# Kernel tuning notes

Hardware: AMD Instinct MI355X
Metric: run time of the kernel (lower is better)

Reference implementation:

```python
import jax, jax.numpy as jnp
import numpy as np

B, S, D_IN, D_H = 16, 4096, 512, 512

def setup_inputs() -> dict:
    key = jax.random.key(0)
    ks = jax.random.split(key, 8)
    inp = {
        "input": jax.random.normal(ks[0], (B, D_IN), dtype=jnp.float32),
        "context": jax.random.normal(ks[1], (B, S, D_IN), dtype=jnp.float32),
        "mask": jax.random.bernoulli(ks[2], 0.2, (B, S)),
        # parameters (torch nn.Linear layout: W [out,in], b [out])
        "W_in": jax.random.normal(ks[3], (D_H, D_IN), dtype=jnp.float32) / np.sqrt(D_IN),
        "b_in": jax.random.normal(ks[4], (D_H,), dtype=jnp.float32) * 0.01,
        "W_ctx": jax.random.normal(ks[5], (D_H, D_IN), dtype=jnp.float32) / np.sqrt(D_IN),
        "b_ctx": jax.random.normal(ks[6], (D_H,), dtype=jnp.float32) * 0.01,
        "v": jax.random.normal(ks[7], (D_H,), dtype=jnp.float32),
    }
    return inp


def reference(input, context, mask, W_in, b_in, W_ctx, b_ctx, v):
    # inp: [B, H] projected decoder state
    inp = input @ W_in.T + b_in
    # ctx: [B, S, H] projected context (this is what the torch code matmuls
    # with the softmax weights, i.e. hidden lives in hidden_dim space)
    ctx = context @ W_ctx.T + b_ctx
    # additive (Bahdanau) scores: v . tanh(inp + ctx) -> [B, S]
    scores = jnp.einsum("h,bsh->bs", v, jnp.tanh(inp[:, None, :] + ctx))
    # masked positions get -inf so they receive zero softmax weight
    scores = jnp.where(mask, -jnp.inf, scores)
    attn = jax.nn.softmax(scores, axis=-1)  # [B, S]
    # weighted sum of projected context: [B, H]
    hidden = jnp.einsum("bsh,bs->bh", ctx, attn)
    return hidden, attn
```

## Files before the change

### kernel.cpp

```cpp
#include <hip/hip_runtime.h>
#include <hip/hip_bf16.h>

#define B_  16
#define S_  4096
#define DIN 512
#define DH  512

typedef _Float16 f16x8 __attribute__((ext_vector_type(8)));
typedef float    f32x4 __attribute__((ext_vector_type(4)));


__device__ __forceinline__ float fast_tanh(float x) {
    float e = __expf(2.f * x);
    return 1.f - 2.f * __builtin_amdgcn_rcpf(e + 1.f);
}

__device__ __forceinline__ void gload_lds16(const void* g, void* l) {
    __builtin_amdgcn_global_load_lds(
        (const __attribute__((address_space(1))) void*)g,
        (__attribute__((address_space(3))) void*)l, 16, 0, 0);
}

__device__ __forceinline__ int mask_at(const void* mask, int isByte, int idx) {
    return isByte ? (int)((const unsigned char*)mask)[idx]
                  : ((const int*)mask)[idx];
}

__global__ void prep_kernel(const float* __restrict__ input,
                            const float* __restrict__ W_in,
                            const float* __restrict__ b_in,
                            const float* __restrict__ W_ctx,
                            const float* __restrict__ b_ctx,
                            const void*  __restrict__ mask,
                            _Float16* __restrict__ W16,
                            float* __restrict__ addv,
                            float* __restrict__ zeroRegion,
                            int* __restrict__ maskflag) {
    int blk = blockIdx.x;
    int tid = threadIdx.x;
    if (blk < 256) {
        int base = blk * 1024 + tid * 4;
        float4 wv = *(const float4*)(W_ctx + base);
        union { _Float16 f[4]; ushort4 u; } cv;
        cv.f[0] = (_Float16)wv.x; cv.f[1] = (_Float16)wv.y;
        cv.f[2] = (_Float16)wv.z; cv.f[3] = (_Float16)wv.w;
        *(ushort4*)(W16 + base) = cv.u;
    } else if (blk < 288) {
        int t = blk - 256;
        int b = t >> 1;
        int h = ((t & 1) << 8) + tid;
        __shared__ float inrow[DIN];
        inrow[tid]       = input[b * DIN + tid];
        inrow[tid + 256] = input[b * DIN + tid + 256];
        __syncthreads();
        const float* wr = W_in + (size_t)h * DIN;
        float acc = 0.f;
        for (int k = 0; k < DIN; k += 4) {
            float4 w4 = *(const float4*)(wr + k);
            acc += w4.x * inrow[k] + w4.y * inrow[k + 1]
                 + w4.z * inrow[k + 2] + w4.w * inrow[k + 3];
        }
        addv[b * DH + h] = acc + b_in[h] + b_ctx[h];
    } else if (blk == 288) {
        const uint4* m4 = (const uint4*)mask;
        unsigned int orw = 0;
#pragma unroll
        for (int it = 0; it < 16; ++it) {
            uint4 w = m4[it * 256 + tid];
            orw |= (w.x | w.y | w.z | w.w);
        }
        int found = ((orw & 0xFFFFFF00u) != 0) ? 1 : 0;
        __shared__ int f;
        if (tid == 0) f = 0;
        __syncthreads();
        if (found) atomicOr(&f, 1);
        __syncthreads();
        if (tid == 0) maskflag[0] = f;
    } else {
        int base = (blk - 289) * 4096;
#pragma unroll
        for (int it = 0; it < 16; ++it)
            zeroRegion[base + it * 256 + tid] = 0.f;
    }
}

__global__ __launch_bounds__(512, 4)
void score_kernel(const float* __restrict__ context,
                  const _Float16* __restrict__ W16,
                  const float* __restrict__ addv,
                  const float* __restrict__ v,
                  float* __restrict__ scores) {
    __shared__ float    As[2][4096];
    __shared__ _Float16 Bs[2][8192];

    const int tid  = threadIdx.x;
    const int wave = tid >> 6;
    const int lane = tid & 63;
    const int l15  = lane & 15;
    const int q    = lane >> 4;
    const int sg   = wave >> 1;
    const int ng   = wave & 1;

    const int b  = blockIdx.x >> 6;
    const int st = (blockIdx.x & 63) >> 1;
    const int nt = blockIdx.x & 1;
    const int s0 = st * 128;
    const int n0 = nt * 256;

    const float* ctxA = context + ((size_t)b * S_ + s0) * DIN;

#define STAGE(kc_, buf_)                                                       \
    {                                                                          \
        _Pragma("unroll")                                                      \
        for (int u = 0; u < 4; ++u) {                                          \
            int id = wave * 4 + u;                                             \
            if (id < 16) {                                                     \
                int jm = id >> 1, p = id & 1;                                  \
                const float* g = ctxA + (size_t)(jm * 16 + l15) * DIN +        \
                                 (kc_) * 32 + q * 8 + p * 4;                   \
                gload_lds16(g, &As[buf_][jm * 512 + p * 256]);                 \
            } else {                                                           \
                int jn = id - 16;                                              \
                const _Float16* g = W16 +                                      \
                    (size_t)(n0 + jn * 16 + l15) * DIN + (kc_) * 32 + q * 8;   \
                gload_lds16(g, &Bs[buf_][jn * 512]);                           \
            }                                                                  \
        }                                                                      \
    }

    f32x4 acc[2][8];
#pragma unroll
    for (int jm = 0; jm < 2; ++jm)
#pragma unroll
        for (int jn = 0; jn < 8; ++jn) acc[jm][jn] = (f32x4){0.f, 0.f, 0.f, 0.f};

    STAGE(0, 0);

    for (int kc = 0; kc < 16; ++kc) {
        __syncthreads();
        int buf = kc & 1;
        if (kc + 1 < 16) STAGE(kc + 1, (kc + 1) & 1);

        f16x8 afr[2];
#pragma unroll
        for (int jm = 0; jm < 2; ++jm) {
            int jma = sg * 2 + jm;
            float4 x0 = *(const float4*)&As[buf][jma * 512 + lane * 4];
            float4 x1 = *(const float4*)&As[buf][jma * 512 + 256 + lane * 4];
            f16x8 t;
            t[0] = (_Float16)x0.x; t[1] = (_Float16)x0.y;
            t[2] = (_Float16)x0.z; t[3] = (_Float16)x0.w;
            t[4] = (_Float16)x1.x; t[5] = (_Float16)x1.y;
            t[6] = (_Float16)x1.z; t[7] = (_Float16)x1.w;
            afr[jm] = t;
        }
#pragma unroll
        for (int jn = 0; jn < 8; ++jn) {
            int jna = ng * 8 + jn;
            f16x8 bf = *(const f16x8*)&Bs[buf][jna * 512 + q * 128 + l15 * 8];
            acc[0][jn] = __builtin_amdgcn_mfma_f32_16x16x32_f16(afr[0], bf, acc[0][jn], 0, 0, 0);
            acc[1][jn] = __builtin_amdgcn_mfma_f32_16x16x32_f16(afr[1], bf, acc[1][jn], 0, 0, 0);
        }
    }

    const float* avb = addv + b * DH;
    float rowsum[2][4] = {{0.f,0.f,0.f,0.f},{0.f,0.f,0.f,0.f}};
#pragma unroll
    for (int jn = 0; jn < 8; ++jn) {
        int n = n0 + (ng * 8 + jn) * 16 + l15;
        float av = avb[n];
        float vv = v[n];
#pragma unroll
        for (int jm = 0; jm < 2; ++jm)
#pragma unroll
            for (int r = 0; r < 4; ++r)
                rowsum[jm][r] += vv * fast_tanh(acc[jm][jn][r] + av);
    }
#pragma unroll
    for (int jm = 0; jm < 2; ++jm)
#pragma unroll
        for (int r = 0; r < 4; ++r) {
            float s = rowsum[jm][r];
            s += __shfl_xor(s, 1, 16);
            s += __shfl_xor(s, 2, 16);
            s += __shfl_xor(s, 4, 16);
            s += __shfl_xor(s, 8, 16);
            if (l15 == 0) {
                int srow = s0 + (sg * 2 + jm) * 16 + q * 4 + r;
                atomicAdd(&scores[b * S_ + srow], s);
            }
        }
}

__global__ __launch_bounds__(256)
void stats_kernel(const float* __restrict__ scores,
                  const void* __restrict__ mask,
                  const int* __restrict__ maskflag,
                  float* __restrict__ stats) {
    __shared__ float rbuf[8];
    int b = blockIdx.x, tid = threadIdx.x;
    int wv = tid >> 6, ln = tid & 63;
    int isByte = maskflag[0];
    const float* sr = scores + b * S_;

    float mx = -__builtin_inff();
    float vals[16];
#pragma unroll
    for (int it = 0; it < 16; ++it) {
        int s = it * 256 + tid;
        float x = mask_at(mask, isByte, b * S_ + s) ? -__builtin_inff() : sr[s];
        vals[it] = x;
        mx = fmaxf(mx, x);
    }
    for (int o = 1; o < 64; o <<= 1) mx = fmaxf(mx, __shfl_xor(mx, o, 64));
    if (ln == 0) rbuf[wv] = mx;
    __syncthreads();
    mx = fmaxf(fmaxf(rbuf[0], rbuf[1]), fmaxf(rbuf[2], rbuf[3]));

    float sum = 0.f;
#pragma unroll
    for (int it = 0; it < 16; ++it) sum += __expf(vals[it] - mx);
    for (int o = 1; o < 64; o <<= 1) sum += __shfl_xor(sum, o, 64);
    __syncthreads();
    if (ln == 0) rbuf[4 + wv] = sum;
    __syncthreads();
    if (tid == 0) {
        sum = rbuf[4] + rbuf[5] + rbuf[6] + rbuf[7];
        stats[b * 2]     = mx;
        stats[b * 2 + 1] = 1.f / sum;
    }
}

__global__ __launch_bounds__(256)
void attnwsum_kernel(const float* __restrict__ scores,
                     const float* __restrict__ context,
                     const void* __restrict__ mask,
                     const int* __restrict__ maskflag,
                     const float* __restrict__ stats,
                     float* __restrict__ attn,
                     float* __restrict__ wsum) {
    __shared__ int   selIdx[256];
    __shared__ float selW[256];
    __shared__ int   selCount;

    int b  = blockIdx.x >> 4;
    int c0 = (blockIdx.x & 15) * 256;
    int tid = threadIdx.x;
    int isByte = maskflag[0];
    float mx  = stats[b * 2];
    float inv = stats[b * 2 + 1];

    if (tid == 0) selCount = 0;
    __syncthreads();

    int s = c0 + tid;
    int idx = b * S_ + s;
    float sc = mask_at(mask, isByte, idx) ? -__builtin_inff() : scores[idx];
    float p = __expf(sc - mx) * inv;
    attn[idx] = p;
    if (p > 1e-9f) {
        int k = atomicAdd(&selCount, 1);
        selIdx[k] = s;
        selW[k]  = p;
    }
    __syncthreads();

    int cnt = selCount;
    if (cnt == 0) return;
    const float* cb = context + (size_t)b * S_ * DIN;
    float a00 = 0.f, a01 = 0.f, a10 = 0.f, a11 = 0.f;
    float a20 = 0.f, a21 = 0.f, a30 = 0.f, a31 = 0.f;
    int i = 0;
    for (; i + 4 <= cnt; i += 4) {
        const float* c0p = cb + (size_t)selIdx[i]     * DIN;
        const float* c1p = cb + (size_t)selIdx[i + 1] * DIN;
        const float* c2p = cb + (size_t)selIdx[i + 2] * DIN;
        const float* c3p = cb + (size_t)selIdx[i + 3] * DIN;
        float w0 = selW[i], w1 = selW[i + 1], w2 = selW[i + 2], w3 = selW[i + 3];
        a00 += w0 * c0p[tid]; a01 += w0 * c0p[tid + 256];
        a10 += w1 * c1p[tid]; a11 += w1 * c1p[tid + 256];
        a20 += w2 * c2p[tid]; a21 += w2 * c2p[tid + 256];
        a30 += w3 * c3p[tid]; a31 += w3 * c3p[tid + 256];
    }
    float acc0 = (a00 + a10) + (a20 + a30);
    float acc1 = (a01 + a11) + (a21 + a31);
    for (; i < cnt; ++i) {
        const float* cr = cb + (size_t)selIdx[i] * DIN;
        float w = selW[i];
        acc0 += w * cr[tid];
        acc1 += w * cr[tid + 256];
    }
    atomicAdd(&wsum[b * DIN + tid], acc0);
    atomicAdd(&wsum[b * DIN + tid + 256], acc1);
}

__global__ __launch_bounds__(256)
void hidden_kernel(const float* __restrict__ W_ctx,
                   const float* __restrict__ b_ctx,
                   const float* __restrict__ wsum,
                   float* __restrict__ hidden) {
    int b = blockIdx.x >> 1;
    int tid = threadIdx.x;
    int h = ((blockIdx.x & 1) << 8) + tid;
    __shared__ float wrow[DIN];
    wrow[tid]       = wsum[b * DIN + tid];
    wrow[tid + 256] = wsum[b * DIN + tid + 256];
    __syncthreads();
    const float* wr = W_ctx + (size_t)h * DIN;
    float acc = 0.f;
    for (int k = 0; k < DIN; k += 4) {
        float4 w4 = *(const float4*)(wr + k);
        acc += w4.x * wrow[k] + w4.y * wrow[k + 1]
             + w4.z * wrow[k + 2] + w4.w * wrow[k + 3];
    }
    hidden[b * DH + h] = acc + b_ctx[h];
}

extern "C" void kernel_launch(void* const* d_in, const int* in_sizes, int n_in,
                              void* d_out, int out_size, void* d_ws, size_t ws_size,
                              hipStream_t stream) {
    const float* input   = (const float*)d_in[0];
    const float* context = (const float*)d_in[1];
    const void*  mask    = d_in[2];
    const float* W_in    = (const float*)d_in[3];
    const float* b_in    = (const float*)d_in[4];
    const float* W_ctx   = (const float*)d_in[5];
    const float* b_ctx   = (const float*)d_in[6];
    const float* v       = (const float*)d_in[7];

    char* ws = (char*)d_ws;
    _Float16* W16   = (_Float16*)ws;
    float* addv     = (float*)(ws + 524288);
    float* scores   = (float*)(ws + 557056);
    float* wsum     = (float*)(ws + 819200);
    int*   maskflag = (int*)(ws + 851968);
    float* stats    = (float*)(ws + 852096);

    float* hidden = (float*)d_out;
    float* attn   = (float*)d_out + B_ * DH;

    prep_kernel<<<355, 256, 0, stream>>>(input, W_in, b_in, W_ctx, b_ctx, mask,
                                         W16, addv, scores , maskflag);
    score_kernel<<<1024, 512, 0, stream>>>(context, W16, addv, v, scores);
    stats_kernel<<<B_, 256, 0, stream>>>(scores, mask, maskflag, stats);
    attnwsum_kernel<<<B_ * 16, 256, 0, stream>>>(scores, context, mask, maskflag,
                                                 stats, attn, wsum);
    hidden_kernel<<<B_ * 2, 256, 0, stream>>>(W_ctx, b_ctx, wsum, hidden);
}
```

Measured before the change: 300.8 us.

## Retile score GEMM with register-staged fp16 A, XCD-aware mapping, wider softmax kernels

The score GEMM now uses 256-thread blocks with 128x128 tiles and a 4x4 MFMA tile per wave. The fp32 context is loaded into registers and converted to fp16 once on the way into LDS, instead of being converted at every fragment read. Block indices are remapped so that blocks sharing the same context rows land on the same XCD, which should help L2 reuse. The stats kernel moves to 1024 threads and attnwsum to 64-row chunks for more parallelism. The register-staged A path raises register pressure, and the smaller N tile doubles how often context is read.

```diff
diff --git a/kernel.cpp b/kernel.cpp
--- a/kernel.cpp
+++ b/kernel.cpp
@@ -7,6 +7,7 @@
 #define DH  512
 
 typedef _Float16 f16x8 __attribute__((ext_vector_type(8)));
+typedef _Float16 f16x4 __attribute__((ext_vector_type(4)));
 typedef float    f32x4 __attribute__((ext_vector_type(4)));
 
 
@@ -84,14 +85,14 @@
     }
 }
 
-__global__ __launch_bounds__(512, 4)
+__global__ __launch_bounds__(256)
 void score_kernel(const float* __restrict__ context,
                   const _Float16* __restrict__ W16,
                   const float* __restrict__ addv,
                   const float* __restrict__ v,
                   float* __restrict__ scores) {
-    __shared__ float    As[2][4096];
-    __shared__ _Float16 Bs[2][8192];
+    __shared__ __align__(16) _Float16 As[2][4096];
+    __shared__ __align__(16) _Float16 Bs[2][4096];
 
     const int tid  = threadIdx.x;
     const int wave = tid >> 6;
@@ -101,83 +102,108 @@
     const int sg   = wave >> 1;
     const int ng   = wave & 1;
 
-    const int b  = blockIdx.x >> 6;
-    const int st = (blockIdx.x & 63) >> 1;
-    const int nt = blockIdx.x & 1;
-    const int s0 = st * 128;
-    const int n0 = nt * 256;
+    const int xcd  = blockIdx.x & 7;
+    const int slot = blockIdx.x >> 3;
+    const int nt   = slot & 3;
+    const int g    = (slot >> 2) * 8 + xcd;
+    const int b    = g >> 5;
+    const int st   = g & 31;
+    const int s0   = st * 128;
+    const int n0   = nt * 128;
 
     const float* ctxA = context + ((size_t)b * S_ + s0) * DIN;
 
-#define STAGE(kc_, buf_)                                                       \
+#define STAGE_B(kc_, buf_)                                                     \
+    {                                                                          \
+        _Pragma("unroll")                                                      \
+        for (int u = 0; u < 2; ++u) {                                          \
+            int jn = wave * 2 + u;                                             \
+            const _Float16* gp = W16 +                                         \
+                (size_t)(n0 + jn * 16 + l15) * DIN + (kc_) * 32 + q * 8;       \
+            gload_lds16(gp, &Bs[buf_][jn * 512]);                              \
+        }                                                                      \
+    }
+
+    float4 areg[4];
+#define LOADA(kc_)                                                             \
     {                                                                          \
         _Pragma("unroll")                                                      \
         for (int u = 0; u < 4; ++u) {                                          \
-            int id = wave * 4 + u;                                             \
-            if (id < 16) {                                                     \
-                int jm = id >> 1, p = id & 1;                                  \
-                const float* g = ctxA + (size_t)(jm * 16 + l15) * DIN +        \
-                                 (kc_) * 32 + q * 8 + p * 4;                   \
-                gload_lds16(g, &As[buf_][jm * 512 + p * 256]);                 \
-            } else {                                                           \
-                int jn = id - 16;                                              \
-                const _Float16* g = W16 +                                      \
-                    (size_t)(n0 + jn * 16 + l15) * DIN + (kc_) * 32 + q * 8;   \
-                gload_lds16(g, &Bs[buf_][jn * 512]);                           \
-            }                                                                  \
+            int sgi = u * 256 + tid;                                           \
+            int row = sgi >> 3, p = sgi & 7;                                   \
+            areg[u] = *(const float4*)(ctxA + (size_t)row * DIN +              \
+                                       (kc_) * 32 + p * 4);                    \
         }                                                                      \
     }
 
-    f32x4 acc[2][8];
-#pragma unroll
-    for (int jm = 0; jm < 2; ++jm)
-#pragma unroll
-        for (int jn = 0; jn < 8; ++jn) acc[jm][jn] = (f32x4){0.f, 0.f, 0.f, 0.f};
-
-    STAGE(0, 0);
+#define WRITEA(buf_)                                                           \
+    {                                                                          \
+        _Pragma("unroll")                                                      \
+        for (int u = 0; u < 4; ++u) {                                          \
+            int sgi = u * 256 + tid;                                           \
+            int row = sgi >> 3, p = sgi & 7;                                   \
+            int off = (row >> 4) * 512 + (p >> 1) * 128 + (row & 15) * 8 +     \
+                      (p & 1) * 4;                                             \
+            f16x4 hv;                                                          \
+            hv[0] = (_Float16)areg[u].x; hv[1] = (_Float16)areg[u].y;          \
+            hv[2] = (_Float16)areg[u].z; hv[3] = (_Float16)areg[u].w;          \
+            *(f16x4*)&As[buf_][off] = hv;                                      \
+        }                                                                      \
+    }
+
+    f32x4 acc[4][4];
+#pragma unroll
+    for (int jm = 0; jm < 4; ++jm)
+#pragma unroll
+        for (int jn = 0; jn < 4; ++jn) acc[jm][jn] = (f32x4){0.f, 0.f, 0.f, 0.f};
+
+    STAGE_B(0, 0);
+    LOADA(0);
+    WRITEA(0);
+    __syncthreads();
 
     for (int kc = 0; kc < 16; ++kc) {
+        const int cur = kc & 1, nxt = cur ^ 1;
+        if (kc + 1 < 16) {
+            STAGE_B(kc + 1, nxt);
+            LOADA(kc + 1);
+        }
+
+        f16x8 afr[4], bfr[4];
+#pragma unroll
+        for (int jm = 0; jm < 4; ++jm)
+            afr[jm] = *(const f16x8*)&As[cur][(sg * 4 + jm) * 512 + q * 128 + l15 * 8];
+#pragma unroll
+        for (int jn = 0; jn < 4; ++jn)
+            bfr[jn] = *(const f16x8*)&Bs[cur][(ng * 4 + jn) * 512 + q * 128 + l15 * 8];
+
+#pragma unroll
+        for (int jn = 0; jn < 4; ++jn)
+#pragma unroll
+            for (int jm = 0; jm < 4; ++jm)
+                acc[jm][jn] = __builtin_amdgcn_mfma_f32_16x16x32_f16(
+                    afr[jm], bfr[jn], acc[jm][jn], 0, 0, 0);
+
+        if (kc + 1 < 16) WRITEA(nxt);
         __syncthreads();
-        int buf = kc & 1;
-        if (kc + 1 < 16) STAGE(kc + 1, (kc + 1) & 1);
-
-        f16x8 afr[2];
-#pragma unroll
-        for (int jm = 0; jm < 2; ++jm) {
-            int jma = sg * 2 + jm;
-            float4 x0 = *(const float4*)&As[buf][jma * 512 + lane * 4];
-            float4 x1 = *(const float4*)&As[buf][jma * 512 + 256 + lane * 4];
-            f16x8 t;
-            t[0] = (_Float16)x0.x; t[1] = (_Float16)x0.y;
-            t[2] = (_Float16)x0.z; t[3] = (_Float16)x0.w;
-            t[4] = (_Float16)x1.x; t[5] = (_Float16)x1.y;
-            t[6] = (_Float16)x1.z; t[7] = (_Float16)x1.w;
-            afr[jm] = t;
-        }
-#pragma unroll
-        for (int jn = 0; jn < 8; ++jn) {
-            int jna = ng * 8 + jn;
-            f16x8 bf = *(const f16x8*)&Bs[buf][jna * 512 + q * 128 + l15 * 8];
-            acc[0][jn] = __builtin_amdgcn_mfma_f32_16x16x32_f16(afr[0], bf, acc[0][jn], 0, 0, 0);
-            acc[1][jn] = __builtin_amdgcn_mfma_f32_16x16x32_f16(afr[1], bf, acc[1][jn], 0, 0, 0);
-        }
     }
 
     const float* avb = addv + b * DH;
-    float rowsum[2][4] = {{0.f,0.f,0.f,0.f},{0.f,0.f,0.f,0.f}};
-#pragma unroll
-    for (int jn = 0; jn < 8; ++jn) {
-        int n = n0 + (ng * 8 + jn) * 16 + l15;
+    float rowsum[4][4] = {{0.f,0.f,0.f,0.f},{0.f,0.f,0.f,0.f},
+                          {0.f,0.f,0.f,0.f},{0.f,0.f,0.f,0.f}};
+#pragma unroll
+    for (int jn = 0; jn < 4; ++jn) {
+        int n = n0 + (ng * 4 + jn) * 16 + l15;
         float av = avb[n];
         float vv = v[n];
 #pragma unroll
-        for (int jm = 0; jm < 2; ++jm)
+        for (int jm = 0; jm < 4; ++jm)
 #pragma unroll
             for (int r = 0; r < 4; ++r)
                 rowsum[jm][r] += vv * fast_tanh(acc[jm][jn][r] + av);
     }
 #pragma unroll
-    for (int jm = 0; jm < 2; ++jm)
+    for (int jm = 0; jm < 4; ++jm)
 #pragma unroll
         for (int r = 0; r < 4; ++r) {
             float s = rowsum[jm][r];
@@ -186,28 +212,28 @@
             s += __shfl_xor(s, 4, 16);
             s += __shfl_xor(s, 8, 16);
             if (l15 == 0) {
-                int srow = s0 + (sg * 2 + jm) * 16 + q * 4 + r;
+                int srow = s0 + (sg * 4 + jm) * 16 + q * 4 + r;
                 atomicAdd(&scores[b * S_ + srow], s);
             }
         }
 }
 
-__global__ __launch_bounds__(256)
+__global__ __launch_bounds__(1024)
 void stats_kernel(const float* __restrict__ scores,
                   const void* __restrict__ mask,
                   const int* __restrict__ maskflag,
                   float* __restrict__ stats) {
-    __shared__ float rbuf[8];
+    __shared__ float rbuf[32];
     int b = blockIdx.x, tid = threadIdx.x;
     int wv = tid >> 6, ln = tid & 63;
     int isByte = maskflag[0];
     const float* sr = scores + b * S_;
 
     float mx = -__builtin_inff();
-    float vals[16];
-#pragma unroll
-    for (int it = 0; it < 16; ++it) {
-        int s = it * 256 + tid;
+    float vals[4];
+#pragma unroll
+    for (int it = 0; it < 4; ++it) {
+        int s = it * 1024 + tid;
         float x = mask_at(mask, isByte, b * S_ + s) ? -__builtin_inff() : sr[s];
         vals[it] = x;
         mx = fmaxf(mx, x);
@@ -215,19 +241,23 @@
     for (int o = 1; o < 64; o <<= 1) mx = fmaxf(mx, __shfl_xor(mx, o, 64));
     if (ln == 0) rbuf[wv] = mx;
     __syncthreads();
-    mx = fmaxf(fmaxf(rbuf[0], rbuf[1]), fmaxf(rbuf[2], rbuf[3]));
+    float m2 = rbuf[0];
+#pragma unroll
+    for (int i = 1; i < 16; ++i) m2 = fmaxf(m2, rbuf[i]);
+    mx = m2;
 
     float sum = 0.f;
 #pragma unroll
-    for (int it = 0; it < 16; ++it) sum += __expf(vals[it] - mx);
+    for (int it = 0; it < 4; ++it) sum += __expf(vals[it] - mx);
     for (int o = 1; o < 64; o <<= 1) sum += __shfl_xor(sum, o, 64);
-    __syncthreads();
-    if (ln == 0) rbuf[4 + wv] = sum;
+    if (ln == 0) rbuf[16 + wv] = sum;
     __syncthreads();
     if (tid == 0) {
-        sum = rbuf[4] + rbuf[5] + rbuf[6] + rbuf[7];
+        float t = 0.f;
+#pragma unroll
+        for (int i = 0; i < 16; ++i) t += rbuf[16 + i];
         stats[b * 2]     = mx;
-        stats[b * 2 + 1] = 1.f / sum;
+        stats[b * 2 + 1] = 1.f / t;
     }
 }
 
@@ -239,12 +269,12 @@
                      const float* __restrict__ stats,
                      float* __restrict__ attn,
                      float* __restrict__ wsum) {
-    __shared__ int   selIdx[256];
-    __shared__ float selW[256];
+    __shared__ int   selIdx[64];
+    __shared__ float selW[64];
     __shared__ int   selCount;
 
-    int b  = blockIdx.x >> 4;
-    int c0 = (blockIdx.x & 15) * 256;
+    int b  = blockIdx.x >> 6;
+    int c0 = (blockIdx.x & 63) * 64;
     int tid = threadIdx.x;
     int isByte = maskflag[0];
     float mx  = stats[b * 2];
@@ -253,15 +283,17 @@
     if (tid == 0) selCount = 0;
     __syncthreads();
 
-    int s = c0 + tid;
-    int idx = b * S_ + s;
-    float sc = mask_at(mask, isByte, idx) ? -__builtin_inff() : scores[idx];
-    float p = __expf(sc - mx) * inv;
-    attn[idx] = p;
-    if (p > 1e-9f) {
-        int k = atomicAdd(&selCount, 1);
-        selIdx[k] = s;
-        selW[k]  = p;
+    if (tid < 64) {
+        int s = c0 + tid;
+        int idx = b * S_ + s;
+        float sc = mask_at(mask, isByte, idx) ? -__builtin_inff() : scores[idx];
+        float p = __expf(sc - mx) * inv;
+        attn[idx] = p;
+        if (p > 1e-9f) {
+            int k = atomicAdd(&selCount, 1);
+            selIdx[k] = s;
+            selW[k]  = p;
+        }
     }
     __syncthreads();
 
@@ -341,9 +373,9 @@
 
     prep_kernel<<<355, 256, 0, stream>>>(input, W_in, b_in, W_ctx, b_ctx, mask,
                                          W16, addv, scores , maskflag);
-    score_kernel<<<1024, 512, 0, stream>>>(context, W16, addv, v, scores);
-    stats_kernel<<<B_, 256, 0, stream>>>(scores, mask, maskflag, stats);
-    attnwsum_kernel<<<B_ * 16, 256, 0, stream>>>(scores, context, mask, maskflag,
+    score_kernel<<<2048, 256, 0, stream>>>(context, W16, addv, v, scores);
+    stats_kernel<<<B_, 1024, 0, stream>>>(scores, mask, maskflag, stats);
+    attnwsum_kernel<<<B_ * 64, 256, 0, stream>>>(scores, context, mask, maskflag,
                                                  stats, attn, wsum);
     hidden_kernel<<<B_ * 2, 256, 0, stream>>>(W_ctx, b_ctx, wsum, hidden);
 }
```

Measured after the change: 312.7 us. +4.0%, slower.
